# Kernel tuning notes

Measured on AMD Instinct MI355X. Metric: run time of the kernel, lower is better.

Reference implementation:

```python
import jax, jax.numpy as jnp
import numpy as np

B, T, F, H, BB = 256, 512, 5, 512, 128  # batch, seq, features, hidden, cfc backbone units


def lecun_tanh(x):
    return 1.7159 * jnp.tanh(0.666 * x)


def setup_inputs() -> dict:
    key = jax.random.key(0)
    ks = jax.random.split(key, 18)
    def p(k, shape, fan_in):
        lim = 1.0 / np.sqrt(fan_in)
        return jax.random.uniform(k, shape, jnp.float32, -lim, lim)
    return {
        "x": jax.random.normal(ks[0], (B, T, F), jnp.float32),
        # ncps LSTMCell: input_map Linear(F,4H,bias=True), recurrent_map Linear(H,4H,bias=False)
        "lstm_Wi": p(ks[1], (4 * H, F), F),
        "lstm_bi": p(ks[2], (4 * H,), F),
        "lstm_Wh": p(ks[3], (4 * H, H), H),
        # CfCCell backbone: Linear(F+H, BB) + lecun_tanh
        "bb_W": p(ks[4], (BB, F + H), F + H),
        "bb_b": p(ks[5], (BB,), F + H),
        # ff1/ff2/time_a/time_b: Linear(BB, H)
        "ff1_W": p(ks[6], (H, BB), BB), "ff1_b": p(ks[7], (H,), BB),
        "ff2_W": p(ks[8], (H, BB), BB), "ff2_b": p(ks[9], (H,), BB),
        "ta_W": p(ks[10], (H, BB), BB), "ta_b": p(ks[11], (H,), BB),
        "tb_W": p(ks[12], (H, BB), BB), "tb_b": p(ks[13], (H,), BB),
        # heads
        "pred_W": p(ks[14], (2, H), H), "pred_b": p(ks[15], (2,), H),
        "en_W": p(ks[16], (1, H), H), "en_b": p(ks[17], (1,), H),
    }


def _forward(x, lstm_Wi, lstm_bi, lstm_Wh, bb_W, bb_b,
             ff1_W, ff1_b, ff2_W, ff2_b, ta_W, ta_b, tb_W, tb_b,
             pred_W, pred_b, en_W, en_b):
    xt = jnp.swapaxes(x, 0, 1)  # [T, B, F]
    h0 = jnp.zeros((x.shape[0], H), x.dtype)
    c0 = jnp.zeros_like(h0)

    def step(carry, x_t):
        h, c = carry
        # mixed-memory LSTM cell (ncps: forget gate has +1.0 bias)
        z = x_t @ lstm_Wi.T + lstm_bi + h @ lstm_Wh.T  # [B, 4H]
        i, ig, fg, og = jnp.split(z, 4, axis=1)
        c_new = c * jax.nn.sigmoid(fg + 1.0) + jnp.tanh(i) * jax.nn.sigmoid(ig)
        h_lstm = jnp.tanh(c_new) * jax.nn.sigmoid(og)
        # CfC cell (mode=default, ts=1.0)
        feat = lecun_tanh(jnp.concatenate([x_t, h_lstm], axis=1) @ bb_W.T + bb_b)  # [B, BB]
        ff1 = jnp.tanh(feat @ ff1_W.T + ff1_b)
        ff2 = jnp.tanh(feat @ ff2_W.T + ff2_b)
        t_interp = jax.nn.sigmoid((feat @ ta_W.T + ta_b) + (feat @ tb_W.T + tb_b))
        h_new = ff1 * (1.0 - t_interp) + t_interp * ff2
        return (h_new, c_new), h_new

    (h_last, c_last), h_seq = jax.lax.scan(step, (h0, c0), xt)
    h_seq = jnp.swapaxes(h_seq, 0, 1)  # [B, T, H]
    y_pred = h_seq @ pred_W.T + pred_b  # [B, T, 2]
    e_pred = h_seq @ en_W.T + en_b      # [B, T, 1]
    return y_pred, e_pred, h_last, c_last


def reference(x, lstm_Wi, lstm_bi, lstm_Wh, bb_W, bb_b,
              ff1_W, ff1_b, ff2_W, ff2_b, ta_W, ta_b, tb_W, tb_b,
              pred_W, pred_b, en_W, en_b):
    return _forward(x, lstm_Wi, lstm_bi, lstm_Wh, bb_W, bb_b,
                    ff1_W, ff1_b, ff2_W, ff2_b, ta_W, ta_b, tb_W, tb_b,
                    pred_W, pred_b, en_W, en_b)
```

## Files before the change

### kernel.cpp

```cpp
#include <hip/hip_runtime.h>

#define Bn   256
#define Tn   512
#define Fn   5
#define Hn   512
#define BBn  128
#define KSn  544
#define KSP  552
#define BBP  136
#define NC   8
#define WPC  32
#define NWG  (NC*WPC)

typedef __attribute__((ext_vector_type(8))) short bf16x8;
typedef __attribute__((ext_vector_type(4))) float f32x4;
typedef unsigned long long u64;

#define WS_BAR   0
#define WS_PRB   1024
#define WS_DC    2048
#define WS_XCC   4096
#define WS_POK   5120
#define WS_PDT   6144
#define WS_H     24576
#define WS_HL    (WS_H   + Bn*KSn*2)
#define WS_FEAT  (WS_HL  + Bn*KSn*2)
#define WS_WH    (WS_FEAT + Bn*BBn*2)
#define WS_BB    (WS_WH  + 2048*KSn*2)
#define WS_FF    (WS_BB  + 128*KSn*2)

#define LB_A     0
#define LB_WH    (LB_A + 32*KSP*2)
#define LB_FF    (LB_WH + 64*KSP*2)
#define DYN_LDS  (LB_FF + 64*BBP*2)

#define YO 0
#define EO (Bn*Tn*2)
#define HO (EO + Bn*Tn)
#define CO (HO + Bn*Hn)

__device__ __forceinline__ unsigned short f2bf(float f) {
  union { float f; unsigned u; } v; v.f = f;
  unsigned r = v.u + 0x7FFFu + ((v.u >> 16) & 1u);
  return (unsigned short)(r >> 16);
}
__device__ __forceinline__ float bf2f(unsigned short u) {
  union { unsigned u; float f; } v; v.u = ((unsigned)u) << 16;
  return v.f;
}
__device__ __forceinline__ float sigm(float x) { return 1.f / (1.f + __expf(-x)); }
__device__ __forceinline__ float tanhx(float x) {
  float e = __expf(2.f * x);
  return 1.f - 2.f / (e + 1.f);
}

__device__ __forceinline__ u64 ldq_agent(const void* p) {
  return __hip_atomic_load((const u64*)p, __ATOMIC_RELAXED, __HIP_MEMORY_SCOPE_AGENT);
}
__device__ __forceinline__ int ldi_agent(const void* p) {
  return __hip_atomic_load((const int*)p, __ATOMIC_RELAXED, __HIP_MEMORY_SCOPE_AGENT);
}

__device__ __forceinline__ void l2_add_nr(int* p, int v) {
  asm volatile("global_atomic_add %0, %1, off" :: "v"(p), "v"(v) : "memory");
}
__device__ __forceinline__ int l2_add_ret(int* p, int v) {
  int old;
  asm volatile("global_atomic_add %0, %1, %2, off sc0\n\t"
               "s_waitcnt vmcnt(0)"
               : "=v"(old) : "v"(p), "v"(v) : "memory");
  return old;
}

__global__ void __launch_bounds__(256) prep_weights(
    const float* __restrict__ Wh, const float* __restrict__ Wi, const float* __restrict__ bbW,
    const float* __restrict__ f1W, const float* __restrict__ f2W,
    const float* __restrict__ taW, const float* __restrict__ tbW, char* __restrict__ ws)
{
  unsigned short* wh = (unsigned short*)(ws + WS_WH);
  unsigned short* bb = (unsigned short*)(ws + WS_BB);
  unsigned short* ff = (unsigned short*)(ws + WS_FF);
  const int n1 = 2048 * KSn, n2 = 128 * KSn, n3 = Hn * BBn;
  const int ntot = n1 + n2 + 4 * n3;
  for (int i = blockIdx.x * blockDim.x + threadIdx.x; i < ntot; i += gridDim.x * blockDim.x) {
    if (i < n1) {
      int c = i / KSn, k = i % KSn;
      float v = (k < 512) ? Wh[c * 512 + k] : ((k < 517) ? Wi[c * 5 + (k - 512)] : 0.f);
      wh[i] = f2bf(v);
    } else if (i < n1 + n2) {
      int j = i - n1; int o = j / KSn, k = j % KSn;
      float v = (k < 512) ? bbW[o * 517 + 5 + k] : ((k < 517) ? bbW[o * 517 + (k - 512)] : 0.f);
      bb[j] = f2bf(v);
    } else {
      int j = i - n1 - n2; int m = j / n3; int r = j % n3;
      const float* src = (m == 0) ? f1W : (m == 1) ? f2W : (m == 2) ? taW : tbW;
      ff[j] = f2bf(src[r]);
    }
  }
}

__device__ __forceinline__ void cluster_bar(int* ctr, int target, bool fast) {
  __syncthreads();
  if (threadIdx.x == 0) {
    if (fast) {
      l2_add_nr(ctr, 1);
      int tries = 0;
      while (l2_add_ret(ctr, 0) < target) {
        __builtin_amdgcn_s_sleep(1);
        if (++tries >= (1 << 18)) break;
      }
    } else {
      __threadfence();
      atomicAdd(ctr, 1);
      int tries = 0;
      while (__hip_atomic_load(ctr, __ATOMIC_RELAXED, __HIP_MEMORY_SCOPE_AGENT) < target) {
        __builtin_amdgcn_s_sleep(2);
        if (++tries >= (1 << 18)) break;
      }
      __threadfence();
    }
  }
  __syncthreads();
}

__global__ void __launch_bounds__(256, 1) ebl_main(
    const float* __restrict__ x,   const float* __restrict__ bi,
    const float* __restrict__ bbb, const float* __restrict__ f1b, const float* __restrict__ f2b,
    const float* __restrict__ tab, const float* __restrict__ tbb,
    const float* __restrict__ predW, const float* __restrict__ predb,
    const float* __restrict__ enW,   const float* __restrict__ enb,
    float* __restrict__ out, char* __restrict__ ws)
{
  extern __shared__ char lds[];
  __shared__ float lbuf[4][16][36];
  __shared__ int   pflag;

  unsigned short* hsh = (unsigned short*)(ws + WS_H);
  unsigned short* hls = (unsigned short*)(ws + WS_HL);
  unsigned short* fsh = (unsigned short*)(ws + WS_FEAT);
  const unsigned short* wh  = (const unsigned short*)(ws + WS_WH);
  const unsigned short* bbw = (const unsigned short*)(ws + WS_BB);
  const unsigned short* ffw = (const unsigned short*)(ws + WS_FF);

  const int tid  = threadIdx.x;
  const int lane = tid & 63;
  const int wv   = tid >> 6;
  const int cl   = blockIdx.x & 7;
  const int wg   = blockIdx.x >> 3;
  const int rbase = cl * WPC;
  const int jbase = wg * 16;

  int* cctr = (int*)(ws + WS_BAR) + cl * 32;
  int* pctr = (int*)(ws + WS_PRB) + cl * 32;
  int* dctr = (int*)(ws + WS_DC);
  int* xccb = (int*)(ws + WS_XCC);
  int* pokb = (int*)(ws + WS_POK);
  int* pdat = (int*)(ws + WS_PDT);

  const int l15 = lane & 15;
  const int l4  = lane >> 4;
  const int cc  = tid & 15;
  const int rr  = tid >> 4;

  for (int idx = tid; idx < 64 * 68; idx += 256) {
    int r = idx / 68, ch = idx - r * 68;
    int g = r >> 4, c = r & 15;
    bf16x8 v = *(const bf16x8*)(wh + (g * 512 + jbase + c) * KSn + ch * 8);
    *(bf16x8*)(lds + LB_WH + r * (KSP * 2) + ch * 16) = v;
  }
  for (int idx = tid; idx < 64 * 16; idx += 256) {
    int r = idx >> 4, ch = idx & 15;
    int m = r >> 4, c = r & 15;
    bf16x8 v = *(const bf16x8*)(ffw + m * (Hn * BBn) + (jbase + c) * BBn + ch * 8);
    *(bf16x8*)(lds + LB_FF + r * (BBP * 2) + ch * 16) = v;
  }

  float hp0[8], hp1[8], hpe[8];
  if (wv == 0) {
    #pragma unroll
    for (int j = 0; j < 8; ++j) {
      hp0[j] = predW[lane * 8 + j];
      hp1[j] = predW[512 + lane * 8 + j];
      hpe[j] = enW[lane * 8 + j];
    }
  }
  float biC[4];
  #pragma unroll
  for (int g = 0; g < 4; ++g) biC[g] = bi[g * 512 + jbase + cc];
  const float fb1 = f1b[jbase + cc], fb2v = f2b[jbase + cc];
  const float fta = tab[jbase + cc], ftb = tbb[jbase + cc];
  const float bbB = (wg < 8) ? bbb[wg * 16 + l15] : 0.f;

  float cst0 = 0.f, cst1 = 0.f;

  int xcc;
  asm volatile("s_getreg_b32 %0, hwreg(HW_REG_XCC_ID)" : "=s"(xcc));
  if (tid == 0) { xccb[blockIdx.x] = xcc; pflag = 1; }
  if (tid < Fn) {
    int b = rbase + wg;
    hsh[b * KSn + 512 + tid] = f2bf(x[(b * Tn + 0) * Fn + tid]);
  }
  cluster_bar(dctr, NWG, false);

  int refx = xccb[cl];
  int vx   = xccb[cl + 8 * (tid & 31)];
  const bool fast = (__ballot(vx != refx) == 0ull);

  if (fast) {
    if (tid == 0) pdat[blockIdx.x * 16] = 1000 + blockIdx.x;
    cluster_bar(pctr, WPC, true);
    {
      int g = cl + 8 * (tid & 31);
      if (ldi_agent(&pdat[g * 16]) != 1000 + g) pflag = 0;
    }
    __syncthreads();
    if (tid == 0) pdat[blockIdx.x * 16] = 777000 + blockIdx.x * 3;
    cluster_bar(pctr, 2 * WPC, true);
    {
      int g = cl + 8 * (tid & 31);
      if (ldi_agent(&pdat[g * 16]) != 777000 + g * 3) pflag = 0;
    }
    __syncthreads();
    if (tid == 0) pokb[blockIdx.x] = pflag;
    __syncthreads();
  }
  cluster_bar(dctr, 2 * NWG, false);

  int pv = pokb[cl + 8 * (tid & 31)];
  const bool fastrun = fast && (__ballot(pv == 0) == 0ull);

  int phase = 0;
  for (int t = 0; t < Tn; ++t) {
    if (wv == 0 && t > 0) {
      const int b = rbase + wg;
      u64 q0 = ldq_agent((const char*)hsh + b * (KSn * 2) + lane * 16);
      u64 q1 = ldq_agent((const char*)hsh + b * (KSn * 2) + lane * 16 + 8);
      float s0 = 0.f, s1 = 0.f, se = 0.f;
      #pragma unroll
      for (int j = 0; j < 8; ++j) {
        unsigned short us = (unsigned short)(((j < 4) ? q0 : q1) >> (16 * (j & 3)));
        float hv = bf2f(us);
        s0 += hv * hp0[j]; s1 += hv * hp1[j]; se += hv * hpe[j];
      }
      #pragma unroll
      for (int off = 32; off > 0; off >>= 1) {
        s0 += __shfl_down(s0, off);
        s1 += __shfl_down(s1, off);
        se += __shfl_down(se, off);
      }
      if (lane == 0) {
        out[YO + b * (Tn * 2) + (t - 1) * 2 + 0] = s0 + predb[0];
        out[YO + b * (Tn * 2) + (t - 1) * 2 + 1] = s1 + predb[1];
        out[EO + b * Tn + (t - 1)]               = se + enb[0];
      }
    }
    if (tid < Fn) {
      int b = rbase + wg;
      hls[b * KSn + 512 + tid] = f2bf(x[(b * Tn + t) * Fn + tid]);
    }

    for (int idx = tid; idx < 32 * 136; idx += 256) {
      int r = idx / 136, ch = idx - r * 136;
      u64 v = ldq_agent((const char*)hsh + (rbase + r) * (KSn * 2) + ch * 8);
      *(u64*)(lds + LB_A + r * (KSP * 2) + ch * 8) = v;
    }
    __syncthreads();
    {
      f32x4 acc0 = {0.f, 0.f, 0.f, 0.f}, acc1 = {0.f, 0.f, 0.f, 0.f};
      const char* a0b = lds + LB_A + l15 * (KSP * 2) + l4 * 16;
      const char* a1b = a0b + 16 * (KSP * 2);
      const char* wb  = lds + LB_WH + (wv * 16 + l15) * (KSP * 2) + l4 * 16;
      #pragma unroll
      for (int ks = 0; ks < 17; ++ks) {
        bf16x8 a0 = *(const bf16x8*)(a0b + ks * 64);
        bf16x8 a1 = *(const bf16x8*)(a1b + ks * 64);
        bf16x8 b8 = *(const bf16x8*)(wb + ks * 64);
        acc0 = __builtin_amdgcn_mfma_f32_16x16x32_bf16(a0, b8, acc0, 0, 0, 0);
        acc1 = __builtin_amdgcn_mfma_f32_16x16x32_bf16(a1, b8, acc1, 0, 0, 0);
      }
      *(f32x4*)(&lbuf[wv][l15][l4 * 4])      = acc0;
      *(f32x4*)(&lbuf[wv][l15][16 + l4 * 4]) = acc1;
    }
    __syncthreads();
    {
      float zi0 = lbuf[0][cc][rr]      + biC[0];
      float zg0 = lbuf[1][cc][rr]      + biC[1];
      float zf0 = lbuf[2][cc][rr]      + biC[2];
      float zo0 = lbuf[3][cc][rr]      + biC[3];
      float zi1 = lbuf[0][cc][rr + 16] + biC[0];
      float zg1 = lbuf[1][cc][rr + 16] + biC[1];
      float zf1 = lbuf[2][cc][rr + 16] + biC[2];
      float zo1 = lbuf[3][cc][rr + 16] + biC[3];
      float cn0 = cst0 * sigm(zf0 + 1.f) + tanhx(zi0) * sigm(zg0);
      float cn1 = cst1 * sigm(zf1 + 1.f) + tanhx(zi1) * sigm(zg1);
      float hl0 = tanhx(cn0) * sigm(zo0);
      float hl1 = tanhx(cn1) * sigm(zo1);
      cst0 = cn0; cst1 = cn1;
      const int b0 = rbase + rr, b1 = rbase + rr + 16;
      hls[b0 * KSn + jbase + cc] = f2bf(hl0);
      hls[b1 * KSn + jbase + cc] = f2bf(hl1);
      if (t == Tn - 1) {
        out[CO + b0 * Hn + jbase + cc] = cn0;
        out[CO + b1 * Hn + jbase + cc] = cn1;
      }
    }
    ++phase; cluster_bar(cctr, phase * WPC, fastrun);

    if (wg < 8) {
      for (int idx = tid; idx < 32 * 136; idx += 256) {
        int r = idx / 136, ch = idx - r * 136;
        u64 v = ldq_agent((const char*)hls + (rbase + r) * (KSn * 2) + ch * 8);
        *(u64*)(lds + LB_A + r * (KSP * 2) + ch * 8) = v;
      }
      __syncthreads();
      if (wv < 2) {
        f32x4 accB = {0.f, 0.f, 0.f, 0.f};
        const char* ab = lds + LB_A + (wv * 16 + l15) * (KSP * 2) + l4 * 16;
        const unsigned short* brow = bbw + (wg * 16 + l15) * KSn + l4 * 8;
        #pragma unroll
        for (int ks = 0; ks < 17; ++ks) {
          bf16x8 a  = *(const bf16x8*)(ab + ks * 64);
          bf16x8 b8 = *(const bf16x8*)(brow + ks * 32);
          accB = __builtin_amdgcn_mfma_f32_16x16x32_bf16(a, b8, accB, 0, 0, 0);
        }
        #pragma unroll
        for (int j = 0; j < 4; ++j) {
          float v = accB[j] + bbB;
          v = 1.7159f * tanhx(0.666f * v);
          int b = rbase + wv * 16 + l4 * 4 + j;
          fsh[b * BBn + wg * 16 + l15] = f2bf(v);
        }
      }
    }
    ++phase; cluster_bar(cctr, phase * WPC, fastrun);

    for (int idx = tid; idx < 32 * 32; idx += 256) {
      int r = idx >> 5, ch = idx & 31;
      u64 v = ldq_agent((const char*)fsh + (rbase + r) * (BBn * 2) + ch * 8);
      *(u64*)(lds + LB_A + r * (BBP * 2) + ch * 8) = v;
    }
    __syncthreads();
    {
      f32x4 ac0 = {0.f, 0.f, 0.f, 0.f}, ac1 = {0.f, 0.f, 0.f, 0.f};
      const char* a0b = lds + LB_A + l15 * (BBP * 2) + l4 * 16;
      const char* a1b = a0b + 16 * (BBP * 2);
      const char* wb  = lds + LB_FF + (wv * 16 + l15) * (BBP * 2) + l4 * 16;
      #pragma unroll
      for (int ks = 0; ks < 4; ++ks) {
        bf16x8 a0 = *(const bf16x8*)(a0b + ks * 64);
        bf16x8 a1 = *(const bf16x8*)(a1b + ks * 64);
        bf16x8 b8 = *(const bf16x8*)(wb + ks * 64);
        ac0 = __builtin_amdgcn_mfma_f32_16x16x32_bf16(a0, b8, ac0, 0, 0, 0);
        ac1 = __builtin_amdgcn_mfma_f32_16x16x32_bf16(a1, b8, ac1, 0, 0, 0);
      }
      *(f32x4*)(&lbuf[wv][l15][l4 * 4])      = ac0;
      *(f32x4*)(&lbuf[wv][l15][16 + l4 * 4]) = ac1;
    }
    __syncthreads();
    {
      float p10 = lbuf[0][cc][rr] + fb1,      p20 = lbuf[1][cc][rr] + fb2v;
      float pa0 = lbuf[2][cc][rr] + fta,      pb0 = lbuf[3][cc][rr] + ftb;
      float p11 = lbuf[0][cc][rr + 16] + fb1, p21 = lbuf[1][cc][rr + 16] + fb2v;
      float pa1 = lbuf[2][cc][rr + 16] + fta, pb1 = lbuf[3][cc][rr + 16] + ftb;
      float f10 = tanhx(p10), f20 = tanhx(p20), ti0 = sigm(pa0 + pb0);
      float f11 = tanhx(p11), f21 = tanhx(p21), ti1 = sigm(pa1 + pb1);
      float hn0 = f10 + ti0 * (f20 - f10);
      float hn1 = f11 + ti1 * (f21 - f11);
      const int b0 = rbase + rr, b1 = rbase + rr + 16;
      hsh[b0 * KSn + jbase + cc] = f2bf(hn0);
      hsh[b1 * KSn + jbase + cc] = f2bf(hn1);
      if (t == Tn - 1) {
        out[HO + b0 * Hn + jbase + cc] = hn0;
        out[HO + b1 * Hn + jbase + cc] = hn1;
      }
    }
    if (t + 1 < Tn && tid < Fn) {
      int b = rbase + wg;
      hsh[b * KSn + 512 + tid] = f2bf(x[(b * Tn + t + 1) * Fn + tid]);
    }
    ++phase; cluster_bar(cctr, phase * WPC, fastrun);
  }

  if (wv == 0) {
    const int b = rbase + wg;
    u64 q0 = ldq_agent((const char*)hsh + b * (KSn * 2) + lane * 16);
    u64 q1 = ldq_agent((const char*)hsh + b * (KSn * 2) + lane * 16 + 8);
    float s0 = 0.f, s1 = 0.f, se = 0.f;
    #pragma unroll
    for (int j = 0; j < 8; ++j) {
      unsigned short us = (unsigned short)(((j < 4) ? q0 : q1) >> (16 * (j & 3)));
      float hv = bf2f(us);
      s0 += hv * hp0[j]; s1 += hv * hp1[j]; se += hv * hpe[j];
    }
    #pragma unroll
    for (int off = 32; off > 0; off >>= 1) {
      s0 += __shfl_down(s0, off);
      s1 += __shfl_down(s1, off);
      se += __shfl_down(se, off);
    }
    if (lane == 0) {
      out[YO + b * (Tn * 2) + (Tn - 1) * 2 + 0] = s0 + predb[0];
      out[YO + b * (Tn * 2) + (Tn - 1) * 2 + 1] = s1 + predb[1];
      out[EO + b * Tn + (Tn - 1)]               = se + enb[0];
    }
  }
}

extern "C" void kernel_launch(void* const* d_in, const int* in_sizes, int n_in,
                              void* d_out, int out_size, void* d_ws, size_t ws_size,
                              hipStream_t stream) {
  const float* x   = (const float*)d_in[0];
  const float* Wi  = (const float*)d_in[1];
  const float* bi  = (const float*)d_in[2];
  const float* Wh  = (const float*)d_in[3];
  const float* bbW = (const float*)d_in[4];
  const float* bbb = (const float*)d_in[5];
  const float* f1W = (const float*)d_in[6];
  const float* f1b = (const float*)d_in[7];
  const float* f2W = (const float*)d_in[8];
  const float* f2b = (const float*)d_in[9];
  const float* taW = (const float*)d_in[10];
  const float* tab = (const float*)d_in[11];
  const float* tbW = (const float*)d_in[12];
  const float* tbb = (const float*)d_in[13];
  const float* pW  = (const float*)d_in[14];
  const float* pb  = (const float*)d_in[15];
  const float* eW  = (const float*)d_in[16];
  const float* eb  = (const float*)d_in[17];
  float* out = (float*)d_out;
  char* ws = (char*)d_ws;

  static_assert(DYN_LDS == 123392, "LDS layout");
  (void)hipFuncSetAttribute((const void*)ebl_main,
                            hipFuncAttributeMaxDynamicSharedMemorySize, DYN_LDS);

  hipMemsetAsync(ws, 0, WS_WH, stream);
  prep_weights<<<2048, 256, 0, stream>>>(Wh, Wi, bbW, f1W, f2W, taW, tbW, ws);

  void* args[] = { (void*)&x, (void*)&bi, (void*)&bbb, (void*)&f1b, (void*)&f2b,
                   (void*)&tab, (void*)&tbb, (void*)&pW, (void*)&pb, (void*)&eW,
                   (void*)&eb, (void*)&out, (void*)&ws };
  hipLaunchCooperativeKernel((const void*)ebl_main, dim3(NWG), dim3(256), args,
                             DYN_LDS, stream);
}
```

Baseline: 9.245 ms.

## Compute CfC backbone redundantly per workgroup and replace atomic-counter barrier with flag barrier

Each workgroup now computes the full backbone feature tile for its 32 batch rows locally into LDS instead of having 8 workgroups compute it and share it through global memory. This removes one cluster barrier per timestep, leaving two instead of three. The fast-path barrier is also changed from atomic counter increments to per-workgroup arrival flags, gathered by a leader workgroup that then sets a release flag. The trade-off is redundant backbone MFMA work with global weight loads in every workgroup, more LDS, and a two-hop barrier.

```diff
diff --git a/kernel.cpp b/kernel.cpp
--- a/kernel.cpp
+++ b/kernel.cpp
@@ -25,6 +25,8 @@
 #define WS_H     24576
 #define WS_HL    (WS_H   + Bn*KSn*2)
 #define WS_FEAT  (WS_HL  + Bn*KSn*2)
+#define WS_ARR   WS_FEAT
+#define WS_BFL   (WS_FEAT + 16384)
 #define WS_WH    (WS_FEAT + Bn*BBn*2)
 #define WS_BB    (WS_WH  + 2048*KSn*2)
 #define WS_FF    (WS_BB  + 128*KSn*2)
@@ -32,7 +34,8 @@
 #define LB_A     0
 #define LB_WH    (LB_A + 32*KSP*2)
 #define LB_FF    (LB_WH + 64*KSP*2)
-#define DYN_LDS  (LB_FF + 64*BBP*2)
+#define LB_FT    (LB_FF + 64*BBP*2)
+#define DYN_LDS  (LB_FT + 32*BBP*2)
 
 #define YO 0
 #define EO (Bn*Tn*2)
@@ -60,16 +63,20 @@
 __device__ __forceinline__ int ldi_agent(const void* p) {
   return __hip_atomic_load((const int*)p, __ATOMIC_RELAXED, __HIP_MEMORY_SCOPE_AGENT);
 }
-
-__device__ __forceinline__ void l2_add_nr(int* p, int v) {
-  asm volatile("global_atomic_add %0, %1, off" :: "v"(p), "v"(v) : "memory");
-}
-__device__ __forceinline__ int l2_add_ret(int* p, int v) {
-  int old;
-  asm volatile("global_atomic_add %0, %1, %2, off sc0\n\t"
-               "s_waitcnt vmcnt(0)"
-               : "=v"(old) : "v"(p), "v"(v) : "memory");
-  return old;
+__device__ __forceinline__ void sti_agent(int* p, int v) {
+  __hip_atomic_store(p, v, __ATOMIC_RELAXED, __HIP_MEMORY_SCOPE_AGENT);
+}
+
+__device__ __forceinline__ void stage32(const char* src, char* dst, int tid) {
+  u64 rg[17];
+  #pragma unroll
+  for (int i = 0; i < 17; ++i) rg[i] = ldq_agent(src + (tid + i * 256) * 8);
+  #pragma unroll
+  for (int i = 0; i < 17; ++i) {
+    int idx = tid + i * 256;
+    int r = idx / 136, ch = idx - r * 136;
+    *(u64*)(dst + r * (KSP * 2) + ch * 8) = rg[i];
+  }
 }
 
 __global__ void __launch_bounds__(256) prep_weights(
@@ -99,26 +106,42 @@
   }
 }
 
-__device__ __forceinline__ void cluster_bar(int* ctr, int target, bool fast) {
+__device__ __forceinline__ void flag_bar(int* arr, int* bfl, int wg, int e) {
   __syncthreads();
   if (threadIdx.x == 0) {
-    if (fast) {
-      l2_add_nr(ctr, 1);
+    sti_agent(&arr[wg * 16], e);
+    if (wg == 0) {
       int tries = 0;
-      while (l2_add_ret(ctr, 0) < target) {
+      for (;;) {
+        int mn = 0x7fffffff;
+        #pragma unroll
+        for (int i = 0; i < 32; ++i) { int v = ldi_agent(&arr[i * 16]); mn = (v < mn) ? v : mn; }
+        if (mn >= e || ++tries >= (1 << 15)) break;
         __builtin_amdgcn_s_sleep(1);
-        if (++tries >= (1 << 18)) break;
-      }
+      }
+      sti_agent(bfl, e);
     } else {
-      __threadfence();
-      atomicAdd(ctr, 1);
       int tries = 0;
-      while (__hip_atomic_load(ctr, __ATOMIC_RELAXED, __HIP_MEMORY_SCOPE_AGENT) < target) {
-        __builtin_amdgcn_s_sleep(2);
-        if (++tries >= (1 << 18)) break;
-      }
-      __threadfence();
-    }
+      while (ldi_agent(bfl) < e) {
+        if (++tries >= (1 << 15)) break;
+        __builtin_amdgcn_s_sleep(1);
+      }
+    }
+  }
+  __syncthreads();
+}
+
+__device__ __forceinline__ void slow_bar(int* ctr, int target) {
+  __syncthreads();
+  if (threadIdx.x == 0) {
+    __threadfence();
+    atomicAdd(ctr, 1);
+    int tries = 0;
+    while (__hip_atomic_load(ctr, __ATOMIC_RELAXED, __HIP_MEMORY_SCOPE_AGENT) < target) {
+      __builtin_amdgcn_s_sleep(2);
+      if (++tries >= (1 << 18)) break;
+    }
+    __threadfence();
   }
   __syncthreads();
 }
@@ -137,7 +160,6 @@
 
   unsigned short* hsh = (unsigned short*)(ws + WS_H);
   unsigned short* hls = (unsigned short*)(ws + WS_HL);
-  unsigned short* fsh = (unsigned short*)(ws + WS_FEAT);
   const unsigned short* wh  = (const unsigned short*)(ws + WS_WH);
   const unsigned short* bbw = (const unsigned short*)(ws + WS_BB);
   const unsigned short* ffw = (const unsigned short*)(ws + WS_FF);
@@ -151,11 +173,12 @@
   const int jbase = wg * 16;
 
   int* cctr = (int*)(ws + WS_BAR) + cl * 32;
-  int* pctr = (int*)(ws + WS_PRB) + cl * 32;
   int* dctr = (int*)(ws + WS_DC);
   int* xccb = (int*)(ws + WS_XCC);
   int* pokb = (int*)(ws + WS_POK);
   int* pdat = (int*)(ws + WS_PDT);
+  int* arr  = (int*)(ws + WS_ARR) + cl * (32 * 16);
+  int* bfl  = (int*)(ws + WS_BFL) + cl * 32;
 
   const int l15 = lane & 15;
   const int l4  = lane >> 4;
@@ -189,7 +212,7 @@
   for (int g = 0; g < 4; ++g) biC[g] = bi[g * 512 + jbase + cc];
   const float fb1 = f1b[jbase + cc], fb2v = f2b[jbase + cc];
   const float fta = tab[jbase + cc], ftb = tbb[jbase + cc];
-  const float bbB = (wg < 8) ? bbb[wg * 16 + l15] : 0.f;
+  float bbBv[2] = { bbb[wv * 32 + l15], bbb[wv * 32 + 16 + l15] };
 
   float cst0 = 0.f, cst1 = 0.f;
 
@@ -200,36 +223,35 @@
     int b = rbase + wg;
     hsh[b * KSn + 512 + tid] = f2bf(x[(b * Tn + 0) * Fn + tid]);
   }
-  cluster_bar(dctr, NWG, false);
+  slow_bar(dctr, NWG);
 
   int refx = xccb[cl];
   int vx   = xccb[cl + 8 * (tid & 31)];
   const bool fast = (__ballot(vx != refx) == 0ull);
 
+  int ep = 0;
+  int slowph = 0;
+
   if (fast) {
     if (tid == 0) pdat[blockIdx.x * 16] = 1000 + blockIdx.x;
-    cluster_bar(pctr, WPC, true);
-    {
-      int g = cl + 8 * (tid & 31);
-      if (ldi_agent(&pdat[g * 16]) != 1000 + g) pflag = 0;
-    }
+    flag_bar(arr, bfl, wg, ++ep);
+    { int g = cl + 8 * (tid & 31); if (ldi_agent(&pdat[g * 16]) != 1000 + g) pflag = 0; }
     __syncthreads();
     if (tid == 0) pdat[blockIdx.x * 16] = 777000 + blockIdx.x * 3;
-    cluster_bar(pctr, 2 * WPC, true);
-    {
-      int g = cl + 8 * (tid & 31);
-      if (ldi_agent(&pdat[g * 16]) != 777000 + g * 3) pflag = 0;
-    }
+    flag_bar(arr, bfl, wg, ++ep);
+    { int g = cl + 8 * (tid & 31); if (ldi_agent(&pdat[g * 16]) != 777000 + g * 3) pflag = 0; }
     __syncthreads();
     if (tid == 0) pokb[blockIdx.x] = pflag;
     __syncthreads();
   }
-  cluster_bar(dctr, 2 * NWG, false);
+  slow_bar(dctr, 2 * NWG);
 
   int pv = pokb[cl + 8 * (tid & 31)];
   const bool fastrun = fast && (__ballot(pv == 0) == 0ull);
 
-  int phase = 0;
+  const char* hshB = (const char*)hsh + rbase * (KSn * 2);
+  const char* hlsB = (const char*)hls + rbase * (KSn * 2);
+
   for (int t = 0; t < Tn; ++t) {
     if (wv == 0 && t > 0) {
       const int b = rbase + wg;
@@ -259,11 +281,7 @@
       hls[b * KSn + 512 + tid] = f2bf(x[(b * Tn + t) * Fn + tid]);
     }
 
-    for (int idx = tid; idx < 32 * 136; idx += 256) {
-      int r = idx / 136, ch = idx - r * 136;
-      u64 v = ldq_agent((const char*)hsh + (rbase + r) * (KSn * 2) + ch * 8);
-      *(u64*)(lds + LB_A + r * (KSP * 2) + ch * 8) = v;
-    }
+    stage32(hshB, lds + LB_A, tid);
     __syncthreads();
     {
       f32x4 acc0 = {0.f, 0.f, 0.f, 0.f}, acc1 = {0.f, 0.f, 0.f, 0.f};
@@ -304,51 +322,51 @@
         out[CO + b1 * Hn + jbase + cc] = cn1;
       }
     }
-    ++phase; cluster_bar(cctr, phase * WPC, fastrun);
-
-    if (wg < 8) {
-      for (int idx = tid; idx < 32 * 136; idx += 256) {
-        int r = idx / 136, ch = idx - r * 136;
-        u64 v = ldq_agent((const char*)hls + (rbase + r) * (KSn * 2) + ch * 8);
-        *(u64*)(lds + LB_A + r * (KSP * 2) + ch * 8) = v;
-      }
-      __syncthreads();
-      if (wv < 2) {
-        f32x4 accB = {0.f, 0.f, 0.f, 0.f};
-        const char* ab = lds + LB_A + (wv * 16 + l15) * (KSP * 2) + l4 * 16;
-        const unsigned short* brow = bbw + (wg * 16 + l15) * KSn + l4 * 8;
-        #pragma unroll
-        for (int ks = 0; ks < 17; ++ks) {
-          bf16x8 a  = *(const bf16x8*)(ab + ks * 64);
-          bf16x8 b8 = *(const bf16x8*)(brow + ks * 32);
-          accB = __builtin_amdgcn_mfma_f32_16x16x32_bf16(a, b8, accB, 0, 0, 0);
-        }
-        #pragma unroll
-        for (int j = 0; j < 4; ++j) {
-          float v = accB[j] + bbB;
-          v = 1.7159f * tanhx(0.666f * v);
-          int b = rbase + wv * 16 + l4 * 4 + j;
-          fsh[b * BBn + wg * 16 + l15] = f2bf(v);
-        }
-      }
-    }
-    ++phase; cluster_bar(cctr, phase * WPC, fastrun);
-
-    for (int idx = tid; idx < 32 * 32; idx += 256) {
-      int r = idx >> 5, ch = idx & 31;
-      u64 v = ldq_agent((const char*)fsh + (rbase + r) * (BBn * 2) + ch * 8);
-      *(u64*)(lds + LB_A + r * (BBP * 2) + ch * 8) = v;
+    ++ep;
+    if (fastrun) flag_bar(arr, bfl, wg, ep);
+    else { ++slowph; slow_bar(cctr, slowph * WPC); }
+
+    stage32(hlsB, lds + LB_A, tid);
+    __syncthreads();
+    {
+      f32x4 aB00 = {0.f,0.f,0.f,0.f}, aB01 = {0.f,0.f,0.f,0.f};
+      f32x4 aB10 = {0.f,0.f,0.f,0.f}, aB11 = {0.f,0.f,0.f,0.f};
+      const char* a0b = lds + LB_A + l15 * (KSP * 2) + l4 * 16;
+      const char* a1b = a0b + 16 * (KSP * 2);
+      const char* b0r = (const char*)bbw + (wv * 32 + l15) * (KSn * 2) + l4 * 16;
+      const char* b1r = b0r + 16 * (KSn * 2);
+      #pragma unroll
+      for (int ks = 0; ks < 17; ++ks) {
+        bf16x8 a0 = *(const bf16x8*)(a0b + ks * 64);
+        bf16x8 a1 = *(const bf16x8*)(a1b + ks * 64);
+        bf16x8 b0 = *(const bf16x8*)(b0r + ks * 64);
+        bf16x8 b1 = *(const bf16x8*)(b1r + ks * 64);
+        aB00 = __builtin_amdgcn_mfma_f32_16x16x32_bf16(a0, b0, aB00, 0, 0, 0);
+        aB01 = __builtin_amdgcn_mfma_f32_16x16x32_bf16(a0, b1, aB01, 0, 0, 0);
+        aB10 = __builtin_amdgcn_mfma_f32_16x16x32_bf16(a1, b0, aB10, 0, 0, 0);
+        aB11 = __builtin_amdgcn_mfma_f32_16x16x32_bf16(a1, b1, aB11, 0, 0, 0);
+      }
+      unsigned short* ft = (unsigned short*)(lds + LB_FT);
+      #pragma unroll
+      for (int j = 0; j < 4; ++j) {
+        int r0 = l4 * 4 + j, r1 = 16 + l4 * 4 + j;
+        int c0 = wv * 32 + l15, c1 = wv * 32 + 16 + l15;
+        ft[r0 * BBP + c0] = f2bf(1.7159f * tanhx(0.666f * (aB00[j] + bbBv[0])));
+        ft[r0 * BBP + c1] = f2bf(1.7159f * tanhx(0.666f * (aB01[j] + bbBv[1])));
+        ft[r1 * BBP + c0] = f2bf(1.7159f * tanhx(0.666f * (aB10[j] + bbBv[0])));
+        ft[r1 * BBP + c1] = f2bf(1.7159f * tanhx(0.666f * (aB11[j] + bbBv[1])));
+      }
     }
     __syncthreads();
     {
       f32x4 ac0 = {0.f, 0.f, 0.f, 0.f}, ac1 = {0.f, 0.f, 0.f, 0.f};
-      const char* a0b = lds + LB_A + l15 * (BBP * 2) + l4 * 16;
-      const char* a1b = a0b + 16 * (BBP * 2);
-      const char* wb  = lds + LB_FF + (wv * 16 + l15) * (BBP * 2) + l4 * 16;
+      const char* f0 = lds + LB_FT + l15 * (BBP * 2) + l4 * 16;
+      const char* f1 = f0 + 16 * (BBP * 2);
+      const char* wb = lds + LB_FF + (wv * 16 + l15) * (BBP * 2) + l4 * 16;
       #pragma unroll
       for (int ks = 0; ks < 4; ++ks) {
-        bf16x8 a0 = *(const bf16x8*)(a0b + ks * 64);
-        bf16x8 a1 = *(const bf16x8*)(a1b + ks * 64);
+        bf16x8 a0 = *(const bf16x8*)(f0 + ks * 64);
+        bf16x8 a1 = *(const bf16x8*)(f1 + ks * 64);
         bf16x8 b8 = *(const bf16x8*)(wb + ks * 64);
         ac0 = __builtin_amdgcn_mfma_f32_16x16x32_bf16(a0, b8, ac0, 0, 0, 0);
         ac1 = __builtin_amdgcn_mfma_f32_16x16x32_bf16(a1, b8, ac1, 0, 0, 0);
@@ -378,7 +396,9 @@
       int b = rbase + wg;
       hsh[b * KSn + 512 + tid] = f2bf(x[(b * Tn + t + 1) * Fn + tid]);
     }
-    ++phase; cluster_bar(cctr, phase * WPC, fastrun);
+    ++ep;
+    if (fastrun) flag_bar(arr, bfl, wg, ep);
+    else { ++slowph; slow_bar(cctr, slowph * WPC); }
   }
 
   if (wv == 0) {
@@ -430,7 +450,7 @@
   float* out = (float*)d_out;
   char* ws = (char*)d_ws;
 
-  static_assert(DYN_LDS == 123392, "LDS layout");
+  static_assert(DYN_LDS == 132096, "LDS layout");
   (void)hipFuncSetAttribute((const void*)ebl_main,
                             hipFuncAttributeMaxDynamicSharedMemorySize, DYN_LDS);
 
```

Measured after the change: 17.74 ms. 91.8% more time.
